# Optimization experiments

Measured on AMD Instinct MI355X. Metric: run time of the kernel, lower is better.

The kernel has to match this reference:

```python
import jax, jax.numpy as jnp
import numpy as np

DIM = 1024
N_HEADS = 16
HEAD_DIM = DIM // N_HEADS
SCALE = HEAD_DIM ** -0.5


def setup_inputs() -> dict:
    key = jax.random.key(0)
    k1, k2, k3 = jax.random.split(key, 3)
    inp = jax.random.normal(k1, (8, 1024, DIM), dtype=jnp.float32)
    w_qkv = jax.random.normal(k2, (DIM, 3 * DIM), dtype=jnp.float32) * 0.02
    b_qkv = jnp.zeros((3 * DIM,), dtype=jnp.float32)
    w_proj = jax.random.normal(k3, (DIM, DIM), dtype=jnp.float32) * 0.02
    b_proj = jnp.zeros((DIM,), dtype=jnp.float32)
    return {"inp": inp, "w_qkv": w_qkv, "b_qkv": b_qkv, "w_proj": w_proj, "b_proj": b_proj}


def reference(inp, w_qkv, b_qkv, w_proj, b_proj):
    B, N, D = inp.shape
    qkv = inp @ w_qkv + b_qkv                      # [B, N, 3D]
    qkv = qkv.reshape(B, N, 3, N_HEADS, HEAD_DIM)
    qkv = jnp.transpose(qkv, (2, 0, 3, 1, 4))      # [3, B, H, N, hd]
    q, k, v = qkv[0], qkv[1], qkv[2]
    scores = jnp.einsum('bhqd,bhkd->bhqk', q, k) * SCALE
    attn = jax.nn.softmax(scores, axis=-1)         # dropout p=0 -> identity
    out = jnp.einsum('bhqk,bhkd->bhqd', attn, v)   # [B, H, N, hd]
    out = jnp.transpose(out, (0, 2, 1, 3)).reshape(B, N, D)
    return out @ w_proj + b_proj
```

## Files before the change

kernel.cpp:

```cpp
#include <hip/hip_runtime.h>
#include <hip/hip_bf16.h>
#include <cstdint>


typedef __attribute__((ext_vector_type(8))) short short8;
typedef __attribute__((ext_vector_type(4))) float floatx4;
typedef __attribute__((ext_vector_type(16))) float f32x16;
typedef __attribute__((ext_vector_type(2))) unsigned int uint2v;

__device__ __forceinline__ ushort f2bf(float f) {
    union { float f; uint32_t i; } v; v.f = f;
    uint32_t r = v.i + 0x7fffu + ((v.i >> 16) & 1u);
    return (ushort)(r >> 16);
}
__device__ __forceinline__ uint32_t pack2(float a, float b) {
    return (uint32_t)f2bf(a) | ((uint32_t)f2bf(b) << 16);
}
__device__ __forceinline__ uint32_t cvtpk_bf16(float a, float b) {
    uint32_t r;
    asm("v_cvt_pk_bf16_f32 %0, %1, %2" : "=v"(r) : "v"(a), "v"(b));
    return r;
}
__device__ __forceinline__ void gl2lds16(const void* g, void* lds) {
    __builtin_amdgcn_global_load_lds(
        (const __attribute__((address_space(1))) uint32_t*)(uintptr_t)g,
        (__attribute__((address_space(3))) uint32_t*)(uintptr_t)lds,
        16, 0, 0);
}

__global__ __launch_bounds__(256)
void aprep(const float* __restrict__ in, ushort* __restrict__ ob) {
    const int i = (blockIdx.x * 256 + threadIdx.x) * 8;
    const float4 f0 = *(const float4*)&in[i];
    const float4 f1 = *(const float4*)&in[i + 4];
    uint4 pk;
    pk.x = pack2(f0.x, f0.y); pk.y = pack2(f0.z, f0.w);
    pk.z = pack2(f1.x, f1.y); pk.w = pack2(f1.z, f1.w);
    *(uint4*)&ob[i] = pk;
}

__global__ __launch_bounds__(256)
void wprep(const float* __restrict__ W, ushort* __restrict__ WT,
           int K, int N) {
    __shared__ ushort T[64 * 72];
    const int tid = threadIdx.x;
    const int k0 = blockIdx.y * 64, n0 = blockIdx.x * 64;
#pragma unroll
    for (int i = 0; i < 4; ++i) {
        int c = tid + i * 256;
        int kl = c >> 4, n4 = (c & 15) << 2;
        const float4 f = *(const float4*)&W[(size_t)(k0 + kl) * N + n0 + n4];
        T[(n4 + 0) * 72 + kl] = f2bf(f.x);
        T[(n4 + 1) * 72 + kl] = f2bf(f.y);
        T[(n4 + 2) * 72 + kl] = f2bf(f.z);
        T[(n4 + 3) * 72 + kl] = f2bf(f.w);
    }
    __syncthreads();
#pragma unroll
    for (int i = 0; i < 2; ++i) {
        int c = tid + i * 256;
        int nl = c >> 3, k8 = (c & 7) << 3;
        *(uint4*)&WT[(size_t)(n0 + nl) * K + k0 + k8] =
            *(const uint4*)&T[nl * 72 + k8];
    }
}

template <int MODE, typename OutT>
__global__ __launch_bounds__(256)
void gemm_bt(const ushort* __restrict__ A, const ushort* __restrict__ BT,
             const float* __restrict__ bias, OutT* __restrict__ C,
             ushort* __restrict__ qb, ushort* __restrict__ kb,
             ushort* __restrict__ vb, int M, int Nn, int K) {
    __shared__ ushort As[128 * 64];
    __shared__ ushort Bs[128 * 64];
    const int tid = threadIdx.x;
    const int lane = tid & 63, w = tid >> 6;
    const int wm = w & 1, wn = w >> 1;
    const int l16 = lane & 15, quad = lane >> 4;
    const int m0 = blockIdx.y * 128, n0 = blockIdx.x * 128;
    const int srow = lane >> 3;
    const int cg = (lane & 7) ^ srow;
    const int sx = l16 & 7;

    floatx4 acc[4][4];
#pragma unroll
    for (int i = 0; i < 4; ++i)
#pragma unroll
        for (int j = 0; j < 4; ++j) acc[i][j] = (floatx4)0.f;

    const int nkt = K >> 6;
    for (int kt = 0; kt < nkt; ++kt) {
        __syncthreads();
#pragma unroll
        for (int i = 0; i < 4; ++i) {
            const int row = w * 32 + i * 8 + srow;
            gl2lds16(&BT[(size_t)(n0 + row) * K + kt * 64 + cg * 8],
                     &Bs[(w * 32 + i * 8) * 64]);
            gl2lds16(&A[(size_t)(m0 + row) * K + kt * 64 + cg * 8],
                     &As[(w * 32 + i * 8) * 64]);
        }
        __syncthreads();
#pragma unroll
        for (int kk = 0; kk < 2; ++kk) {
            const int sl = ((kk << 2) | quad) ^ sx;
            short8 af[4], bfr[4];
#pragma unroll
            for (int mi = 0; mi < 4; ++mi)
                af[mi] = *(const short8*)&As[(wm * 64 + mi * 16 + l16) * 64 +
                                             sl * 8];
#pragma unroll
            for (int ni = 0; ni < 4; ++ni)
                bfr[ni] = *(const short8*)&Bs[(wn * 64 + ni * 16 + l16) * 64 +
                                              sl * 8];
#pragma unroll
            for (int mi = 0; mi < 4; ++mi)
#pragma unroll
                for (int ni = 0; ni < 4; ++ni)
                    acc[mi][ni] = __builtin_amdgcn_mfma_f32_16x16x32_bf16(
                        af[mi], bfr[ni], acc[mi][ni], 0, 0, 0);
        }
    }

#pragma unroll
    for (int mi = 0; mi < 4; ++mi) {
#pragma unroll
        for (int ni = 0; ni < 4; ++ni) {
            const int jg = n0 + wn * 64 + ni * 16 + l16;
            const float bv = bias[jg];
#pragma unroll
            for (int r = 0; r < 4; ++r) {
                const int mg = m0 + wm * 64 + mi * 16 + quad * 4 + r;
                const float vout = acc[mi][ni][r] + bv;
                if (MODE == 0) {
                    if (sizeof(OutT) == 4)
                        ((float*)C)[(size_t)mg * Nn + jg] = vout;
                    else
                        ((ushort*)C)[(size_t)mg * Nn + jg] = f2bf(vout);
                } else {
                    const int which = jg >> 10;
                    const int h = (jg & 1023) >> 6;
                    const int d = jg & 63;
                    const int bb = mg >> 10, nn = mg & 1023;
                    if (which == 0)
                        qb[(size_t)((bb * 16 + h) * 1024 + nn) * 64 + d] =
                            f2bf(vout);
                    else if (which == 1)
                        kb[(size_t)((bb * 16 + h) * 1024 + nn) * 64 + d] =
                            f2bf(vout);
                    else
                        vb[((size_t)(bb * 16 + h) * 64 + d) * 1024 + nn] =
                            f2bf(vout);
                }
            }
        }
    }
}

__global__ __launch_bounds__(256, 4)
void attn_kernel(const ushort* __restrict__ q, const ushort* __restrict__ k,
                 const ushort* __restrict__ v, ushort* __restrict__ o) {
    __shared__ ushort Qs[128 * 64];
    __shared__ ushort Ks[64 * 64];
    __shared__ ushort VTs[64 * 64];
    const int tid = threadIdx.x;
    const int lane = tid & 63, w = tid >> 6;
    const int l31 = lane & 31, hi = lane >> 5, l7 = lane & 7;
    const int h = blockIdx.x, qt = blockIdx.y, b = blockIdx.z;
    const size_t head_off = (size_t)(b * 16 + h) * 1024 * 64;
    const ushort* Qp = q + head_off + (size_t)qt * 128 * 64;
    const ushort* Vp = v + head_off;
    const int srow = lane >> 3;
    const int cg = (lane & 7) ^ srow;
    const float CEXP = 0.125f * 1.44269504f;

#pragma unroll
    for (int g = 0; g < 4; ++g)
        gl2lds16(&Qp[(size_t)(w * 32 + g * 8 + srow) * 64 + cg * 8],
                 &Qs[(w * 32 + g * 8) * 64]);
    __syncthreads();

    short8 bq[4];
#pragma unroll
    for (int c = 0; c < 4; ++c)
        bq[c] = *(const short8*)&Qs[(w * 32 + l31) * 64 +
                                    ((2 * c + hi) ^ l7) * 8];

    f32x16 oacc[2];
    oacc[0] = (f32x16)0.f;
    oacc[1] = (f32x16)0.f;
    float ls = 0.f;

    for (int kt = 0; kt < 16; ++kt) {
        __syncthreads();
        const ushort* Kp = k + head_off + (size_t)kt * 64 * 64;
#pragma unroll
        for (int g = 0; g < 2; ++g) {
            gl2lds16(&Kp[(size_t)(w * 16 + g * 8 + srow) * 64 + cg * 8],
                     &Ks[(w * 16 + g * 8) * 64]);
            gl2lds16(&Vp[(size_t)(w * 16 + g * 8 + srow) * 1024 +
                         kt * 64 + cg * 8],
                     &VTs[(w * 16 + g * 8) * 64]);
        }
        __syncthreads();

#pragma unroll
        for (int st = 0; st < 2; ++st) {
            f32x16 sacc = (f32x16)0.f;
#pragma unroll
            for (int c = 0; c < 4; ++c) {
                short8 ak = *(const short8*)&Ks[(st * 32 + l31) * 64 +
                                                ((2 * c + hi) ^ l7) * 8];
                sacc = __builtin_amdgcn_mfma_f32_32x32x16_bf16(
                    ak, bq[c], sacc, 0, 0, 0);
            }
            uint32_t wd[8];
#pragma unroll
            for (int i = 0; i < 8; ++i) {
                const float e0 = __builtin_amdgcn_exp2f(sacc[2 * i] * CEXP);
                const float e1 = __builtin_amdgcn_exp2f(sacc[2 * i + 1] * CEXP);
                ls += e0 + e1;
                wd[i] = cvtpk_bf16(e0, e1);
            }
            short8 ap[2];
#pragma unroll
            for (int c2 = 0; c2 < 2; ++c2) {
                uint2v sA = __builtin_amdgcn_permlane32_swap(
                    wd[4 * c2 + 0], wd[4 * c2 + 2], false, false);
                uint2v sB = __builtin_amdgcn_permlane32_swap(
                    wd[4 * c2 + 1], wd[4 * c2 + 3], false, false);
                union { uint32_t u[4]; short8 s; } t;
                t.u[0] = sA[0]; t.u[1] = sB[0];
                t.u[2] = sA[1]; t.u[3] = sB[1];
                ap[c2] = t.s;
            }
#pragma unroll
            for (int dt = 0; dt < 2; ++dt)
#pragma unroll
                for (int c2 = 0; c2 < 2; ++c2) {
                    short8 bv = *(const short8*)&VTs[
                        (dt * 32 + l31) * 64 +
                        ((st * 4 + c2 * 2 + hi) ^ l7) * 8];
                    oacc[dt] = __builtin_amdgcn_mfma_f32_32x32x16_bf16(
                        ap[c2], bv, oacc[dt], 0, 0, 0);
                }
        }
    }

    ls += __shfl_xor(ls, 32, 64);
    const float inv = 1.f / ls;

#pragma unroll
    for (int r = 0; r < 16; ++r) {
        const int qout = (r & 3) + ((r >> 2) << 3) + (hi << 2);
        const float iq = __shfl(inv, qout, 64);
        const int n = qt * 128 + w * 32 + qout;
#pragma unroll
        for (int dt = 0; dt < 2; ++dt)
            o[((size_t)(b * 1024 + n)) * 1024 + h * 64 + dt * 32 + l31] =
                f2bf(oacc[dt][r] * iq);
    }
}

extern "C" void kernel_launch(void* const* d_in, const int* in_sizes, int n_in,
                              void* d_out, int out_size, void* d_ws,
                              size_t ws_size, hipStream_t stream) {
    const void *inp = d_in[0], *w_qkv = d_in[1], *b_qkv = d_in[2],
               *w_proj = d_in[3], *b_proj = d_in[4];
    for (int i = 0; i < n_in; ++i) {
        switch (in_sizes[i]) {
            case 8 * 1024 * 1024: inp    = d_in[i]; break;
            case 3 * 1024 * 1024: w_qkv  = d_in[i]; break;
            case 3072:            b_qkv  = d_in[i]; break;
            case 1024 * 1024:     w_proj = d_in[i]; break;
            case 1024:            b_proj = d_in[i]; break;
        }
    }
    float* out = (float*)d_out;

    char* ws = (char*)d_ws;
    ushort* qb  = (ushort*)(ws);
    ushort* kb  = (ushort*)(ws + (size_t)16 * 1024 * 1024);
    ushort* vbT = (ushort*)(ws + (size_t)32 * 1024 * 1024);
    ushort* ob  = (ushort*)(ws + (size_t)48 * 1024 * 1024);
    ushort* wqkvT  = ob;
    ushort* wprojT = qb;
    ushort* abf = (ushort*)d_out;

    aprep<<<8 * 1024 * 1024 / (256 * 8), 256, 0, stream>>>(
        (const float*)inp, abf);
    wprep<<<dim3(3072 / 64, 1024 / 64), 256, 0, stream>>>(
        (const float*)w_qkv, wqkvT, 1024, 3072);

    gemm_bt<1, ushort><<<dim3(3072 / 128, 8192 / 128), 256, 0, stream>>>(
        abf, wqkvT, (const float*)b_qkv, (ushort*)nullptr, qb, kb, vbT,
        8192, 3072, 1024);

    attn_kernel<<<dim3(16, 8, 8), 256, 0, stream>>>(qb, kb, vbT, ob);

    wprep<<<dim3(1024 / 64, 1024 / 64), 256, 0, stream>>>(
        (const float*)w_proj, wprojT, 1024, 1024);

    gemm_bt<0, float><<<dim3(1024 / 128, 8192 / 128), 256, 0, stream>>>(
        ob, wprojT, (const float*)b_proj, out, nullptr, nullptr, nullptr,
        8192, 1024, 1024);
}
```

Baseline: 252.0 us.

## Replace QKV GEMM with 256x256-tile 8-wave ping-pong pipelined kernel

Adds a new GEMM kernel that uses 256x256 output tiles, 512 threads and 128KB of dynamic LDS, double-buffered by k-tile and split into quadrants. Staging of the next quadrant is interleaved with MFMA on the current one, using barriers and setprio. The QKV projection now uses it in place of the 128x128 gemm_bt. The aim is more data reuse per LDS load and better overlap of global loads with compute. In exchange, the grid is smaller (384 blocks), register pressure is higher, and the kernel carries many barriers.

Result: slower. 264.1 us (+4.8%).

```diff
diff --git a/kernel.cpp b/kernel.cpp
--- a/kernel.cpp
+++ b/kernel.cpp
@@ -156,6 +156,169 @@
     }
 }
 
+#define STAGE8(mat, half, kt) do {                                            \
+    const ushort* _src = (mat) ? BT : A;                                      \
+    const int _b0 = ((mat) ? n0 : m0) + (half) * 128;                         \
+    ushort* _d = &lds[((((kt) & 1) * 2 + (mat)) * 2 + (half)) * 8192];        \
+    _Pragma("unroll")                                                         \
+    for (int g = 0; g < 2; ++g)                                               \
+        gl2lds16(&_src[(size_t)(_b0 + w * 16 + g * 8 + srow) * K +            \
+                       (kt) * 64 + cg * 8],                                   \
+                 &_d[(w * 16 + g * 8) * 64]);                                 \
+} while (0)
+
+#define LDA8(mq, s) do {                                                      \
+    _Pragma("unroll")                                                         \
+    for (int mi = 0; mi < 4; ++mi)                                            \
+        _Pragma("unroll")                                                     \
+        for (int kk = 0; kk < 2; ++kk)                                        \
+            af[mi][kk] = *(const short8*)&lds[                                \
+                (((s) * 2 + 0) * 2 + (mq)) * 8192 +                           \
+                (wqm * 64 + mi * 16 + l16) * 64 +                             \
+                ((((kk << 2) | quad) ^ sx) << 3)];                            \
+} while (0)
+
+#define LDB8(nq, s) do {                                                      \
+    _Pragma("unroll")                                                         \
+    for (int ni = 0; ni < 2; ++ni)                                            \
+        _Pragma("unroll")                                                     \
+        for (int kk = 0; kk < 2; ++kk)                                        \
+            bf[ni][kk] = *(const short8*)&lds[                                \
+                (((s) * 2 + 1) * 2 + (nq)) * 8192 +                           \
+                (wqn * 32 + ni * 16 + l16) * 64 +                             \
+                ((((kk << 2) | quad) ^ sx) << 3)];                            \
+} while (0)
+
+#define MMA8(mq, nq) do {                                                     \
+    __builtin_amdgcn_s_setprio(1);                                            \
+    _Pragma("unroll")                                                         \
+    for (int kk = 0; kk < 2; ++kk)                                            \
+        _Pragma("unroll")                                                     \
+        for (int mi = 0; mi < 4; ++mi)                                        \
+            _Pragma("unroll")                                                 \
+            for (int ni = 0; ni < 2; ++ni)                                    \
+                acc[mq][nq][mi][ni] =                                         \
+                    __builtin_amdgcn_mfma_f32_16x16x32_bf16(                  \
+                        af[mi][kk], bf[ni][kk], acc[mq][nq][mi][ni],          \
+                        0, 0, 0);                                             \
+    __builtin_amdgcn_s_setprio(0);                                            \
+} while (0)
+
+#define BAR8() __builtin_amdgcn_s_barrier()
+#define WLGKM8() do {                                                         \
+    asm volatile("s_waitcnt lgkmcnt(0)" ::: "memory");                        \
+    __builtin_amdgcn_sched_barrier(0);                                        \
+} while (0)
+
+template <int MODE, typename OutT>
+__global__ __launch_bounds__(512, 2)
+void gemm8p(const ushort* __restrict__ A, const ushort* __restrict__ BT,
+            const float* __restrict__ bias, OutT* __restrict__ C,
+            ushort* __restrict__ qb, ushort* __restrict__ kb,
+            ushort* __restrict__ vb, int M, int Nn, int K) {
+    extern __shared__ ushort lds[];
+    const int tid = threadIdx.x;
+    const int lane = tid & 63, w = tid >> 6;
+    const int wqm = w & 1, wqn = w >> 1;
+    const int l16 = lane & 15, quad = lane >> 4;
+    const int srow = lane >> 3;
+    const int cg = (lane & 7) ^ srow;
+    const int sx = l16 & 7;
+    const int m0 = blockIdx.y * 256, n0 = blockIdx.x * 256;
+
+    floatx4 acc[2][2][4][2];
+#pragma unroll
+    for (int a = 0; a < 2; ++a)
+#pragma unroll
+        for (int b = 0; b < 2; ++b)
+#pragma unroll
+            for (int c = 0; c < 4; ++c)
+#pragma unroll
+                for (int d = 0; d < 2; ++d) acc[a][b][c][d] = (floatx4)0.f;
+
+    short8 af[4][2], bf[2][2];
+
+    const int nkt = K >> 6, niter = nkt >> 1;
+
+    STAGE8(0, 0, 0); STAGE8(1, 0, 0); STAGE8(0, 1, 0); STAGE8(1, 1, 0);
+    STAGE8(0, 0, 1); STAGE8(1, 1, 1);
+    asm volatile("s_waitcnt vmcnt(4)" ::: "memory");
+    BAR8();
+
+    for (int i = 0; i < niter; ++i) {
+        const int t = 2 * i;
+        const bool more2 = (t + 2 < nkt), more3 = (t + 3 < nkt);
+        LDA8(0, 0); LDB8(0, 0);
+        STAGE8(0, 1, t + 1);
+        BAR8(); WLGKM8(); MMA8(0, 0); BAR8();
+        LDB8(1, 0);
+        STAGE8(1, 0, t + 1);
+        BAR8(); WLGKM8(); MMA8(0, 1); BAR8();
+        LDA8(1, 0);
+        if (more2) STAGE8(0, 0, t + 2);
+        BAR8(); WLGKM8(); MMA8(1, 1); BAR8();
+        LDB8(0, 0);
+        if (more2) {
+            STAGE8(1, 1, t + 2);
+            asm volatile("s_waitcnt vmcnt(4)" ::: "memory");
+        } else {
+            asm volatile("s_waitcnt vmcnt(0)" ::: "memory");
+        }
+        BAR8(); WLGKM8(); MMA8(1, 0); BAR8();
+        LDA8(0, 1); LDB8(0, 1);
+        if (more2) STAGE8(0, 1, t + 2);
+        BAR8(); WLGKM8(); MMA8(0, 0); BAR8();
+        LDB8(1, 1);
+        if (more2) STAGE8(1, 0, t + 2);
+        BAR8(); WLGKM8(); MMA8(0, 1); BAR8();
+        LDA8(1, 1);
+        if (more3) STAGE8(0, 0, t + 3);
+        BAR8(); WLGKM8(); MMA8(1, 1); BAR8();
+        LDB8(0, 1);
+        if (more3) STAGE8(1, 1, t + 3);
+        if (more2) asm volatile("s_waitcnt vmcnt(4)" ::: "memory");
+        BAR8(); WLGKM8(); MMA8(1, 0); BAR8();
+    }
+
+#pragma unroll
+    for (int mq = 0; mq < 2; ++mq)
+#pragma unroll
+        for (int nq = 0; nq < 2; ++nq)
+#pragma unroll
+            for (int ni = 0; ni < 2; ++ni) {
+                const int jg = n0 + nq * 128 + wqn * 32 + ni * 16 + l16;
+                const float bv = bias[jg];
+#pragma unroll
+                for (int mi = 0; mi < 4; ++mi)
+#pragma unroll
+                    for (int r = 0; r < 4; ++r) {
+                        const int mg = m0 + mq * 128 + wqm * 64 + mi * 16 +
+                                       quad * 4 + r;
+                        const float vout = acc[mq][nq][mi][ni][r] + bv;
+                        if (MODE == 0) {
+                            if (sizeof(OutT) == 4)
+                                ((float*)C)[(size_t)mg * Nn + jg] = vout;
+                            else
+                                ((ushort*)C)[(size_t)mg * Nn + jg] = f2bf(vout);
+                        } else {
+                            const int which = jg >> 10;
+                            const int h = (jg & 1023) >> 6;
+                            const int d = jg & 63;
+                            const int bb = mg >> 10, nn = mg & 1023;
+                            if (which == 0)
+                                qb[(size_t)((bb * 16 + h) * 1024 + nn) * 64 +
+                                   d] = f2bf(vout);
+                            else if (which == 1)
+                                kb[(size_t)((bb * 16 + h) * 1024 + nn) * 64 +
+                                   d] = f2bf(vout);
+                            else
+                                vb[((size_t)(bb * 16 + h) * 64 + d) * 1024 +
+                                   nn] = f2bf(vout);
+                        }
+                    }
+            }
+}
+
 __global__ __launch_bounds__(256, 4)
 void attn_kernel(const ushort* __restrict__ q, const ushort* __restrict__ k,
                  const ushort* __restrict__ v, ushort* __restrict__ o) {
@@ -286,12 +449,15 @@
     ushort* wprojT = qb;
     ushort* abf = (ushort*)d_out;
 
+    hipFuncSetAttribute(reinterpret_cast<const void*>(&gemm8p<1, ushort>),
+                        hipFuncAttributeMaxDynamicSharedMemorySize, 131072);
+
     aprep<<<8 * 1024 * 1024 / (256 * 8), 256, 0, stream>>>(
         (const float*)inp, abf);
     wprep<<<dim3(3072 / 64, 1024 / 64), 256, 0, stream>>>(
         (const float*)w_qkv, wqkvT, 1024, 3072);
 
-    gemm_bt<1, ushort><<<dim3(3072 / 128, 8192 / 128), 256, 0, stream>>>(
+    gemm8p<1, ushort><<<dim3(3072 / 256, 8192 / 256), 512, 131072, stream>>>(
         abf, wqkvT, (const float*)b_qkv, (ushort*)nullptr, qb, kb, vbT,
         8192, 3072, 1024);
 
```

## Fuse all stages into one persistent megakernel with grid barriers

Applied to the files above, without the earlier changes.

Replaces the six separate launches (input cast, two weight transposes, QKV GEMM, attention, projection GEMM) with one persistent 768-block kernel. Each phase loops over virtual block indices, with a software grid barrier on a counter placed in the output buffer between phases. This removes launch gaps and lets the weight prep overlap with the input cast. It also adds s_setprio hints around the MFMA bursts in attention. The risks are barrier spin cost, uneven attention work (2048 tiles over 768 blocks), lower attention occupancy from the shared 32KB LDS and 3-block launch bound, and reliance on all 768 blocks being resident at once.

Result: slower. 445.9 us (+76.9%).

```diff
diff --git a/kernel.cpp b/kernel.cpp
--- a/kernel.cpp
+++ b/kernel.cpp
@@ -28,9 +28,30 @@
         16, 0, 0);
 }
 
-__global__ __launch_bounds__(256)
-void aprep(const float* __restrict__ in, ushort* __restrict__ ob) {
-    const int i = (blockIdx.x * 256 + threadIdx.x) * 8;
+__device__ __forceinline__ void gridbar(unsigned* cnt, unsigned nblk) {
+    unsigned* gen = cnt + 32;
+    __syncthreads();
+    if (threadIdx.x == 0) {
+        __threadfence();
+        unsigned g = __hip_atomic_load(gen, __ATOMIC_RELAXED,
+                                       __HIP_MEMORY_SCOPE_AGENT);
+        if (atomicAdd(cnt, 1u) == nblk - 1u) {
+            atomicExch(cnt, 0u);
+            __threadfence();
+            atomicAdd(gen, 1u);
+        } else {
+            do { __builtin_amdgcn_s_sleep(32); }
+            while (__hip_atomic_load(gen, __ATOMIC_RELAXED,
+                                     __HIP_MEMORY_SCOPE_AGENT) == g);
+        }
+        __threadfence();
+    }
+    __syncthreads();
+}
+
+__device__ __forceinline__ void aprep_dev(int vb, const float* __restrict__ in,
+                                          ushort* ob) {
+    const int i = (vb * 256 + (int)threadIdx.x) * 8;
     const float4 f0 = *(const float4*)&in[i];
     const float4 f1 = *(const float4*)&in[i + 4];
     uint4 pk;
@@ -39,12 +60,12 @@
     *(uint4*)&ob[i] = pk;
 }
 
-__global__ __launch_bounds__(256)
-void wprep(const float* __restrict__ W, ushort* __restrict__ WT,
-           int K, int N) {
-    __shared__ ushort T[64 * 72];
+__device__ __forceinline__ void wprep_dev(ushort* SM, int k0, int n0,
+                                          const float* __restrict__ W,
+                                          ushort* WT, int K, int N) {
+    ushort* T = SM;
     const int tid = threadIdx.x;
-    const int k0 = blockIdx.y * 64, n0 = blockIdx.x * 64;
+    __syncthreads();
 #pragma unroll
     for (int i = 0; i < 4; ++i) {
         int c = tid + i * 256;
@@ -66,18 +87,17 @@
 }
 
 template <int MODE, typename OutT>
-__global__ __launch_bounds__(256)
-void gemm_bt(const ushort* __restrict__ A, const ushort* __restrict__ BT,
-             const float* __restrict__ bias, OutT* __restrict__ C,
-             ushort* __restrict__ qb, ushort* __restrict__ kb,
-             ushort* __restrict__ vb, int M, int Nn, int K) {
-    __shared__ ushort As[128 * 64];
-    __shared__ ushort Bs[128 * 64];
+__device__ __forceinline__ void gemm_dev(
+    ushort* SM, int bx, int by, const ushort* __restrict__ A,
+    const ushort* __restrict__ BT, const float* __restrict__ bias, OutT* C,
+    ushort* qb, ushort* kb, ushort* vb, int Nn, int K) {
+    ushort* As = SM;
+    ushort* Bs = SM + 8192;
     const int tid = threadIdx.x;
     const int lane = tid & 63, w = tid >> 6;
     const int wm = w & 1, wn = w >> 1;
     const int l16 = lane & 15, quad = lane >> 4;
-    const int m0 = blockIdx.y * 128, n0 = blockIdx.x * 128;
+    const int m0 = by * 128, n0 = bx * 128;
     const int srow = lane >> 3;
     const int cg = (lane & 7) ^ srow;
     const int sx = l16 & 7;
@@ -156,16 +176,15 @@
     }
 }
 
-__global__ __launch_bounds__(256, 4)
-void attn_kernel(const ushort* __restrict__ q, const ushort* __restrict__ k,
-                 const ushort* __restrict__ v, ushort* __restrict__ o) {
-    __shared__ ushort Qs[128 * 64];
-    __shared__ ushort Ks[64 * 64];
-    __shared__ ushort VTs[64 * 64];
+__device__ __forceinline__ void attn_dev(ushort* SM, int h, int qt, int b,
+                                         const ushort* q, const ushort* k,
+                                         const ushort* v, ushort* o) {
+    ushort* Qs = SM;
+    ushort* Ks = SM + 8192;
+    ushort* VTs = SM + 12288;
     const int tid = threadIdx.x;
     const int lane = tid & 63, w = tid >> 6;
     const int l31 = lane & 31, hi = lane >> 5, l7 = lane & 7;
-    const int h = blockIdx.x, qt = blockIdx.y, b = blockIdx.z;
     const size_t head_off = (size_t)(b * 16 + h) * 1024 * 64;
     const ushort* Qp = q + head_off + (size_t)qt * 128 * 64;
     const ushort* Vp = v + head_off;
@@ -206,6 +225,7 @@
 #pragma unroll
         for (int st = 0; st < 2; ++st) {
             f32x16 sacc = (f32x16)0.f;
+            __builtin_amdgcn_s_setprio(1);
 #pragma unroll
             for (int c = 0; c < 4; ++c) {
                 short8 ak = *(const short8*)&Ks[(st * 32 + l31) * 64 +
@@ -213,6 +233,7 @@
                 sacc = __builtin_amdgcn_mfma_f32_32x32x16_bf16(
                     ak, bq[c], sacc, 0, 0, 0);
             }
+            __builtin_amdgcn_s_setprio(0);
             uint32_t wd[8];
 #pragma unroll
             for (int i = 0; i < 8; ++i) {
@@ -233,6 +254,7 @@
                 t.u[2] = sA[1]; t.u[3] = sB[1];
                 ap[c2] = t.s;
             }
+            __builtin_amdgcn_s_setprio(1);
 #pragma unroll
             for (int dt = 0; dt < 2; ++dt)
 #pragma unroll
@@ -243,6 +265,7 @@
                     oacc[dt] = __builtin_amdgcn_mfma_f32_32x32x16_bf16(
                         ap[c2], bv, oacc[dt], 0, 0, 0);
                 }
+            __builtin_amdgcn_s_setprio(0);
         }
     }
 
@@ -259,6 +282,45 @@
             o[((size_t)(b * 1024 + n)) * 1024 + h * 64 + dt * 32 + l31] =
                 f2bf(oacc[dt][r] * iq);
     }
+}
+
+__global__ __launch_bounds__(256, 3)
+void mega(const float* __restrict__ inp, const float* __restrict__ w_qkv,
+          const float* __restrict__ b_qkv, const float* __restrict__ w_proj,
+          const float* __restrict__ b_proj, float* out,
+          ushort* qb, ushort* kb, ushort* vbT, ushort* ob,
+          ushort* wqkvT, ushort* wprojT, ushort* abf, unsigned* bar) {
+    __shared__ ushort SM[16384];
+    const int NB = 768;
+    const int r = blockIdx.x;
+
+    for (int vb = r; vb < 4864; vb += NB) {
+        if (vb < 4096) aprep_dev(vb, inp, abf);
+        else {
+            const int wb = vb - 4096;
+            wprep_dev(SM, (wb / 48) * 64, (wb % 48) * 64, w_qkv, wqkvT,
+                      1024, 3072);
+        }
+    }
+    gridbar(bar, NB);
+
+    for (int vb = r; vb < 1536; vb += NB)
+        gemm_dev<1, ushort>(SM, vb % 24, vb / 24, abf, wqkvT, b_qkv,
+                            (ushort*)nullptr, qb, kb, vbT, 3072, 1024);
+    gridbar(bar, NB);
+
+    for (int vb = r; vb < 2048; vb += NB)
+        attn_dev(SM, vb & 15, (vb >> 4) & 7, vb >> 7, qb, kb, vbT, ob);
+    gridbar(bar, NB);
+
+    for (int vb = r; vb < 256; vb += NB)
+        wprep_dev(SM, (vb / 16) * 64, (vb % 16) * 64, w_proj, wprojT,
+                  1024, 1024);
+    gridbar(bar, NB);
+
+    for (int vb = r; vb < 512; vb += NB)
+        gemm_dev<0, float>(SM, vb % 8, vb / 8, ob, wprojT, b_proj, out,
+                           nullptr, nullptr, nullptr, 1024, 1024);
 }
 
 extern "C" void kernel_launch(void* const* d_in, const int* in_sizes, int n_in,
@@ -285,22 +347,12 @@
     ushort* wqkvT  = ob;
     ushort* wprojT = qb;
     ushort* abf = (ushort*)d_out;
-
-    aprep<<<8 * 1024 * 1024 / (256 * 8), 256, 0, stream>>>(
-        (const float*)inp, abf);
-    wprep<<<dim3(3072 / 64, 1024 / 64), 256, 0, stream>>>(
-        (const float*)w_qkv, wqkvT, 1024, 3072);
-
-    gemm_bt<1, ushort><<<dim3(3072 / 128, 8192 / 128), 256, 0, stream>>>(
-        abf, wqkvT, (const float*)b_qkv, (ushort*)nullptr, qb, kb, vbT,
-        8192, 3072, 1024);
-
-    attn_kernel<<<dim3(16, 8, 8), 256, 0, stream>>>(qb, kb, vbT, ob);
-
-    wprep<<<dim3(1024 / 64, 1024 / 64), 256, 0, stream>>>(
-        (const float*)w_proj, wprojT, 1024, 1024);
-
-    gemm_bt<0, float><<<dim3(1024 / 128, 8192 / 128), 256, 0, stream>>>(
-        ob, wprojT, (const float*)b_proj, out, nullptr, nullptr, nullptr,
-        8192, 1024, 1024);
-}
+    unsigned* bar = (unsigned*)((char*)d_out + (size_t)16 * 1024 * 1024);
+
+    hipMemsetAsync(bar, 0, 256, stream);
+
+    mega<<<768, 256, 0, stream>>>(
+        (const float*)inp, (const float*)w_qkv, (const float*)b_qkv,
+        (const float*)w_proj, (const float*)b_proj, out,
+        qb, kb, vbT, ob, wqkvT, wprojT, abf, bar);
+}
```
